# Kernel tuning notes

Hardware: AMD Instinct MI355X
Metric: run time of the kernel (lower is better)

## Reference

```python
import jax, jax.numpy as jnp
import numpy as np

N = 2048; E = 65536; T = 6; F_IN = 2
H_ENC = 256; LAT = 128; H_DEC = 256
PRED = 6
MIN_X, MAX_X = 0.0, 1.0
MIN_Y, MAX_Y = 0.0, 1.0
MIN_EW, MAX_EW = 0.0, 0.5
VISUAL_RANGE = 0.5


def setup_inputs() -> dict:
    key = jax.random.key(0)
    ks = jax.random.split(key, 17)
    p = lambda k, shape: jax.random.normal(k, shape, jnp.float32) * 0.05
    return {
        "x_seq": jax.random.uniform(ks[0], (T, N, F_IN), jnp.float32),
        "edge_index_seq": jax.random.randint(ks[1], (T, 2, E), 0, N),
        "edge_weight_seq": jax.random.uniform(ks[2], (T, E), jnp.float32, 1e-3, 1.0),
        "h_enc": jnp.zeros((N, H_ENC), jnp.float32),
        "h_dec": jnp.zeros((N, H_DEC), jnp.float32),
        "enc_Wx": p(ks[3], (3, 2, F_IN, H_ENC)),
        "enc_bx": p(ks[4], (3, H_ENC)),
        "enc_Wh": p(ks[5], (3, 2, H_ENC, H_ENC)),
        "enc_bh": p(ks[6], (3, H_ENC)),
        "enc_lin_W": p(ks[7], (H_ENC, LAT)),
        "enc_lin_b": p(ks[8], (LAT,)),
        "dec_Wx": p(ks[9], (3, 2, LAT, H_DEC)),
        "dec_bx": p(ks[10], (3, H_DEC)),
        "dec_Wh": p(ks[11], (3, 2, H_DEC, H_DEC)),
        "dec_bh": p(ks[12], (3, H_DEC)),
        "dec_lin_W": p(ks[13], (H_DEC, F_IN)),
        "dec_lin_b": p(ks[14], (F_IN,)),
    }


def _sparse_conv_fn(edge_index, edge_weight, n):
    # ChebConv K=2, sym normalization, lambda_max=2 => T1(L_hat) = -D^-1/2 A D^-1/2
    src, dst = edge_index[0], edge_index[1]
    deg = jax.ops.segment_sum(edge_weight, src, num_segments=n)
    dinv = jnp.where(deg > 0, jax.lax.rsqrt(jnp.where(deg > 0, deg, 1.0)), 0.0)
    norm = -dinv[src] * edge_weight * dinv[dst]  # [E]

    def conv(x, W, b):  # W: [2, in, out]
        tx1 = jax.ops.segment_sum(norm[:, None] * x[src], dst, num_segments=n)
        return x @ W[0] + tx1 @ W[1] + b
    return conv


def _dense_conv_fn(y_hat):
    # graph rebuilt from detached predicted coords (radius graph, dense masked form)
    c = jax.lax.stop_gradient(y_hat)
    px = c[:, 0] * (MAX_X - MIN_X) + MIN_X
    py = c[:, 1] * (MAX_Y - MIN_Y) + MIN_Y
    coords = jnp.stack((px, py), axis=1)  # [N, 2]
    d = jnp.linalg.norm(coords[:, None, :] - coords[None, :, :], axis=2)  # [N, N]
    mask = (d < VISUAL_RANGE) & (d > 0)
    w = jnp.where(mask, (d - MIN_EW) / (MAX_EW - MIN_EW), 0.0)
    deg = w.sum(axis=1)
    dinv = jnp.where(deg > 0, jax.lax.rsqrt(jnp.where(deg > 0, deg, 1.0)), 0.0)
    M = -(dinv[:, None] * w) * dinv[None, :]  # scaled-Laplacian off-diagonal

    def conv(x, W, b):
        return x @ W[0] + (M @ x) @ W[1] + b
    return conv


def _gru(conv, x, H, Wx, bx, Wh, bh):
    # GConvGRU gates: each gate = conv_x(X) + conv_h(H)
    z = jax.nn.sigmoid(conv(x, Wx[0], bx[0]) + conv(H, Wh[0], bh[0]))
    r = jax.nn.sigmoid(conv(x, Wx[1], bx[1]) + conv(H, Wh[1], bh[1]))
    h_tilde = jnp.tanh(conv(x, Wx[2], bx[2]) + conv(H * r, Wh[2], bh[2]))
    return z * H + (1.0 - z) * h_tilde


def reference(x_seq, edge_index_seq, edge_weight_seq, h_enc, h_dec,
              enc_Wx, enc_bx, enc_Wh, enc_bh, enc_lin_W, enc_lin_b,
              dec_Wx, dec_bx, dec_Wh, dec_bh, dec_lin_W, dec_lin_b):
    n = x_seq.shape[1]

    def step(conv, x, he, hd):
        he0 = _gru(conv, x, he, enc_Wx, enc_bx, enc_Wh, enc_bh)
        z = jax.nn.relu(he0) @ enc_lin_W + enc_lin_b
        hd0 = _gru(conv, z, hd, dec_Wx, dec_bx, dec_Wh, dec_bh)
        y_hat = jax.nn.relu(hd0) @ dec_lin_W + dec_lin_b
        return y_hat, he0, hd0

    # observed snapshots (sparse edge-list graphs)
    for t in range(x_seq.shape[0]):
        conv = _sparse_conv_fn(edge_index_seq[t], edge_weight_seq[t], n)
        y_hat, h_enc, h_dec = step(conv, x_seq[t], h_enc, h_dec)

    preds = [y_hat]
    for _ in range(PRED - 1):
        conv = _dense_conv_fn(y_hat)
        y_hat, h_enc, h_dec = step(conv, y_hat, h_enc, h_dec)
        preds.append(y_hat)
    return jnp.stack(preds)  # [PRED, N, 2]
```

## Files before the change

kernel.cpp:

```cpp
#include <hip/hip_runtime.h>
#include <math.h>

#define NN 2048
#define EE 65536
#define T_OBS 6
#define FIN 2
#define HE 256
#define LT 128
#define PREDN 6
#define DMM_NZ 8
#define ZR_NZ 4
#define GT_NZ 8
#define LIN_NZ 8

typedef __attribute__((ext_vector_type(8))) short short8v;
typedef __attribute__((ext_vector_type(4))) float float4v;

static __device__ __forceinline__ unsigned short f2bf(float f) {
    union { float f; unsigned u; } v; v.f = f;
    unsigned r = v.u + 0x7fff + ((v.u >> 16) & 1);
    return (unsigned short)(r >> 16);
}

static __device__ __forceinline__ void bfsplit(float f, unsigned short& h,
                                               unsigned short& l) {
    unsigned u = __float_as_uint(f);
    h = (unsigned short)(u >> 16);
    float hf = __uint_as_float(u & 0xffff0000u);
    l = (unsigned short)(__float_as_uint(f - hf) >> 16);
}

static __device__ __forceinline__ float bf2f(unsigned short b) {
    return __uint_as_float(((unsigned)b) << 16);
}

__global__ void k_degcnt_b(const int* __restrict__ ei, const float* __restrict__ ews,
                           float* __restrict__ deg_all, int* __restrict__ cnt_all) {
    int t = blockIdx.y;
    int e = blockIdx.x * blockDim.x + threadIdx.x;
    const int* src = ei + (size_t)t * 2 * EE;
    const int* dst = src + EE;
    const float* ew = ews + (size_t)t * EE;
    if (e < EE) {
        atomicAdd(&deg_all[t * NN + src[e]], ew[e]);
        atomicAdd(&cnt_all[t * NN + dst[e]], 1);
    }
}

__global__ void k_scan_b(const int* __restrict__ cnt_all, const float* __restrict__ deg_all,
                         int* __restrict__ roff_all, int* __restrict__ cur_all,
                         float* __restrict__ dinv_all) {
    __shared__ int part[256];
    int tg = blockIdx.x;
    const int* cnt = cnt_all + tg * NN;
    const float* deg = deg_all + tg * NN;
    int* roff = roff_all + tg * (NN + 1);
    int* cur = cur_all + tg * NN;
    float* dinv = dinv_all + tg * NN;
    int t = threadIdx.x;
#pragma unroll
    for (int i = t; i < NN; i += 256) {
        float d = deg[i];
        dinv[i] = d > 0.f ? 1.f / sqrtf(d) : 0.f;
    }
    int loc[8];
    int s = 0;
#pragma unroll
    for (int i = 0; i < 8; i++) { loc[i] = cnt[t * 8 + i]; s += loc[i]; }
    part[t] = s;
    __syncthreads();
    for (int off = 1; off < 256; off <<= 1) {
        int v = (t >= off) ? part[t - off] : 0;
        __syncthreads();
        part[t] += v;
        __syncthreads();
    }
    int run = (t == 0) ? 0 : part[t - 1];
#pragma unroll
    for (int i = 0; i < 8; i++) {
        int idx = t * 8 + i;
        roff[idx] = run;
        cur[idx] = run;
        run += loc[i];
    }
    if (t == 255) roff[NN] = run;
}

__global__ void k_scatter2_b(const int* __restrict__ ei, const float* __restrict__ ews,
                             const float* __restrict__ dinv_all, int* __restrict__ cur_all,
                             int* __restrict__ csr_src_all, float* __restrict__ csr_nrm_all) {
    int tg = blockIdx.y;
    int e = blockIdx.x * blockDim.x + threadIdx.x;
    const int* src = ei + (size_t)tg * 2 * EE;
    const int* dst = src + EE;
    const float* ew = ews + (size_t)tg * EE;
    const float* dinv = dinv_all + tg * NN;
    if (e < EE) {
        int s = src[e], d = dst[e];
        int p = atomicAdd(&cur_all[tg * NN + d], 1);
        csr_src_all[(size_t)tg * EE + p] = s;
        csr_nrm_all[(size_t)tg * EE + p] = -dinv[s] * ew[e] * dinv[d];
    }
}

__global__ void k_spmm2_b(const int* __restrict__ roff_all, const int* __restrict__ csr_src_all,
                          const float* __restrict__ csr_nrm_all, const float* __restrict__ x_seq,
                          float* __restrict__ aggx_all) {
    int tg = blockIdx.y;
    int nid = blockIdx.x * blockDim.x + threadIdx.x;
    if (nid < NN) {
        const int* roff = roff_all + tg * (NN + 1);
        const int* csr_src = csr_src_all + (size_t)tg * EE;
        const float* csr_nrm = csr_nrm_all + (size_t)tg * EE;
        const float* X = x_seq + (size_t)tg * NN * FIN;
        int s0 = roff[nid], s1 = roff[nid + 1];
        float a0 = 0.f, a1 = 0.f;
        for (int s = s0; s < s1; ++s) {
            int i = csr_src[s]; float w = csr_nrm[s];
            float2 xv = *(const float2*)&X[2 * i];
            a0 = fmaf(w, xv.x, a0);
            a1 = fmaf(w, xv.y, a1);
        }
        aggx_all[(size_t)tg * NN * FIN + 2 * nid] = a0;
        aggx_all[(size_t)tg * NN * FIN + 2 * nid + 1] = a1;
    }
}

template <int F>
__global__ void k_spmm_v(const int* __restrict__ roff, const int* __restrict__ csr_src,
                         const float* __restrict__ csr_nrm,
                         const float* __restrict__ X, float* __restrict__ out) {
    int w = threadIdx.x >> 6, lane = threadIdx.x & 63;
    int nid = (blockIdx.x << 2) + w;
    int c = lane << 2;
    int s0 = roff[nid], s1 = roff[nid + 1];
    float4 acc = make_float4(0.f, 0.f, 0.f, 0.f);
    int s = s0;
    for (; s + 8 <= s1; s += 8) {
        int is[8]; float ws[8];
#pragma unroll
        for (int j = 0; j < 8; j++) { is[j] = csr_src[s + j]; ws[j] = csr_nrm[s + j]; }
        if (c < F) {
            float4 xv[8];
#pragma unroll
            for (int j = 0; j < 8; j++) xv[j] = *(const float4*)&X[(size_t)is[j] * F + c];
#pragma unroll
            for (int j = 0; j < 8; j++) {
                acc.x = fmaf(ws[j], xv[j].x, acc.x);
                acc.y = fmaf(ws[j], xv[j].y, acc.y);
                acc.z = fmaf(ws[j], xv[j].z, acc.z);
                acc.w = fmaf(ws[j], xv[j].w, acc.w);
            }
        }
    }
    for (; s < s1; ++s) {
        int i0 = csr_src[s]; float w0 = csr_nrm[s];
        if (c < F) {
            float4 xv = *(const float4*)&X[(size_t)i0 * F + c];
            acc.x = fmaf(w0, xv.x, acc.x);
            acc.y = fmaf(w0, xv.y, acc.y);
            acc.z = fmaf(w0, xv.z, acc.z);
            acc.w = fmaf(w0, xv.w, acc.w);
        }
    }
    if (c < F) *(float4*)&out[(size_t)nid * F + c] = acc;
}

__global__ void k_ddeg(const float* __restrict__ c, float* __restrict__ dinv) {
    int i = blockIdx.x;
    int t = threadIdx.x;
    float xi = c[2 * i], yi = c[2 * i + 1];
    float s = 0.f;
    for (int j = t; j < NN; j += 256) {
        float dx = xi - c[2 * j], dy = yi - c[2 * j + 1];
        float d = sqrtf(dx * dx + dy * dy);
        if (d > 0.f && d < 0.5f) s += 2.f * d;
    }
    __shared__ float red[256];
    red[t] = s;
    __syncthreads();
    for (int off = 128; off > 0; off >>= 1) {
        if (t < off) red[t] += red[t + off];
        __syncthreads();
    }
    if (t == 0) {
        float d = red[0];
        dinv[i] = d > 0.f ? 1.f / sqrtf(d) : 0.f;
    }
}

__global__ void k_dM(const float* __restrict__ c, const float* __restrict__ dinv,
                     unsigned short* __restrict__ Mb) {
    int idx = blockIdx.x * blockDim.x + threadIdx.x;
    int i = idx >> 11, j = idx & (NN - 1);
    float dx = c[2 * i] - c[2 * j], dy = c[2 * i + 1] - c[2 * j + 1];
    float d = sqrtf(dx * dx + dy * dy);
    float w = (d > 0.f && d < 0.5f) ? 2.f * d : 0.f;
    Mb[idx] = f2bf(-(dinv[i] * w) * dinv[j]);
}

template <int F>
__global__ __launch_bounds__(256) void k_dmm_mf(
    const unsigned short* __restrict__ Mb, const float* __restrict__ X,
    float* __restrict__ pbuf)
{
    __shared__ __align__(16) unsigned short Ms[64][72];
    __shared__ __align__(16) unsigned short Xs[64][72];
    const int tid = threadIdx.x;
    const int wid = tid >> 6, lane = tid & 63;
    const int m0 = blockIdx.x << 6, n0 = blockIdx.y << 6;
    const int kb0 = blockIdx.z << 8;
    const int lr = lane & 15;
    const int kg = lane >> 4;
    float4v acc[4];
#pragma unroll
    for (int t = 0; t < 4; t++) acc[t] = (float4v){0.f, 0.f, 0.f, 0.f};

    for (int kb = kb0; kb < kb0 + 256; kb += 64) {
#pragma unroll
        for (int it = 0; it < 2; it++) {
            int i = tid + it * 256;
            int r = i >> 3, c8 = (i & 7) << 3;
            *(short8v*)&Ms[r][c8] =
                *(const short8v*)&Mb[(size_t)(m0 + r) * NN + kb + c8];
        }
#pragma unroll
        for (int it = 0; it < 2; it++) {
            int i = tid + it * 256;
            int k2 = (i & 31) << 1;
            int n4 = (i >> 5) << 2;
            float4 va = *(const float4*)&X[(size_t)(kb + k2) * F + n0 + n4];
            float4 vb = *(const float4*)&X[(size_t)(kb + k2 + 1) * F + n0 + n4];
            unsigned pk;
            pk = (unsigned)f2bf(va.x) | ((unsigned)f2bf(vb.x) << 16);
            *(unsigned*)&Xs[n4 + 0][k2] = pk;
            pk = (unsigned)f2bf(va.y) | ((unsigned)f2bf(vb.y) << 16);
            *(unsigned*)&Xs[n4 + 1][k2] = pk;
            pk = (unsigned)f2bf(va.z) | ((unsigned)f2bf(vb.z) << 16);
            *(unsigned*)&Xs[n4 + 2][k2] = pk;
            pk = (unsigned)f2bf(va.w) | ((unsigned)f2bf(vb.w) << 16);
            *(unsigned*)&Xs[n4 + 3][k2] = pk;
        }
        __syncthreads();
#pragma unroll
        for (int kh = 0; kh < 2; kh++) {
            int kk = kh * 32 + kg * 8;
            short8v a = *(const short8v*)&Ms[(wid << 4) + lr][kk];
#pragma unroll
            for (int t = 0; t < 4; t++) {
                short8v b = *(const short8v*)&Xs[(t << 4) + lr][kk];
                acc[t] = __builtin_amdgcn_mfma_f32_16x16x32_bf16(a, b, acc[t], 0, 0, 0);
            }
        }
        __syncthreads();
    }
    float* p = pbuf + (size_t)blockIdx.z * NN * F;
#pragma unroll
    for (int t = 0; t < 4; t++)
#pragma unroll
        for (int j = 0; j < 4; j++)
            p[(size_t)(m0 + (wid << 4) + (kg << 2) + j) * F + n0 + (t << 4) + lr] =
                acc[t][j];
}

template <int F, int NZ>
__global__ void k_redks(const float* __restrict__ pbuf, float* __restrict__ out) {
    const int TOT = NN * F / 4;
    int i = blockIdx.x * blockDim.x + threadIdx.x;
    if (i < TOT) {
        const float4* p = (const float4*)pbuf;
        float4 s = p[i];
#pragma unroll
        for (int z = 1; z < NZ; z++) {
            float4 v = p[(size_t)z * TOT + i];
            s.x += v.x; s.y += v.y; s.z += v.z; s.w += v.w;
        }
        ((float4*)out)[i] = s;
    }
}

__global__ void k_dmv2b(const unsigned short* __restrict__ Mb, const float* __restrict__ X,
                        float* __restrict__ out) {
    int i = blockIdx.x;
    int t = threadIdx.x;
    float a0 = 0.f, a1 = 0.f;
    for (int j = t; j < NN; j += 256) {
        float m = bf2f(Mb[(size_t)i * NN + j]);
        a0 = fmaf(m, X[2 * j], a0);
        a1 = fmaf(m, X[2 * j + 1], a1);
    }
    __shared__ float r0[256], r1[256];
    r0[t] = a0;
    r1[t] = a1;
    __syncthreads();
    for (int off = 128; off > 0; off >>= 1) {
        if (t < off) { r0[t] += r0[t + off]; r1[t] += r1[t + off]; }
        __syncthreads();
    }
    if (t == 0) { out[2 * i] = r0[0]; out[2 * i + 1] = r1[0]; }
}

template <bool RELU>
__device__ __forceinline__ void mfma_seg(
    unsigned short (*Ah)[40], unsigned short (*Al)[40],
    unsigned short (*Bh)[40], unsigned short (*Bl)[40],
    const float* __restrict__ A, int lda,
    const float* __restrict__ B, int ldb, int K,
    int m0, int tid, int wid, int lr, int kg, float4v (&acc)[4])
{
    for (int k0 = 0; k0 < K; k0 += 32) {
        {
            int r = tid >> 2, k8 = (tid & 3) << 3;
            const float* ap = &A[(size_t)(m0 + r) * lda + k0 + k8];
            float4 va = *(const float4*)ap;
            float4 vb = *(const float4*)(ap + 4);
            float v[8] = {va.x, va.y, va.z, va.w, vb.x, vb.y, vb.z, vb.w};
            short8v hv, lv;
#pragma unroll
            for (int j = 0; j < 8; j++) {
                float f = RELU ? fmaxf(v[j], 0.f) : v[j];
                unsigned short h, l;
                bfsplit(f, h, l);
                hv[j] = (short)h; lv[j] = (short)l;
            }
            *(short8v*)&Ah[r][k8] = hv;
            *(short8v*)&Al[r][k8] = lv;
        }
        {
            int k2 = (tid & 15) << 1;
            int n4 = (tid >> 4) << 2;
            const float* bp = &B[(size_t)(k0 + k2) * ldb + n4];
            float4 va = *(const float4*)bp;
            float4 vb = *(const float4*)(bp + ldb);
            float v0[4] = {va.x, va.y, va.z, va.w};
            float v1[4] = {vb.x, vb.y, vb.z, vb.w};
#pragma unroll
            for (int j = 0; j < 4; j++) {
                unsigned short h0, l0, h1, l1;
                bfsplit(v0[j], h0, l0);
                bfsplit(v1[j], h1, l1);
                *(unsigned*)&Bh[n4 + j][k2] = (unsigned)h0 | ((unsigned)h1 << 16);
                *(unsigned*)&Bl[n4 + j][k2] = (unsigned)l0 | ((unsigned)l1 << 16);
            }
        }
        __syncthreads();
        short8v ah = *(short8v*)&Ah[(wid << 4) + lr][kg << 3];
        short8v al = *(short8v*)&Al[(wid << 4) + lr][kg << 3];
#pragma unroll
        for (int t = 0; t < 4; t++) {
            short8v bh = *(short8v*)&Bh[(t << 4) + lr][kg << 3];
            short8v bl = *(short8v*)&Bl[(t << 4) + lr][kg << 3];
            acc[t] = __builtin_amdgcn_mfma_f32_16x16x32_bf16(ah, bh, acc[t], 0, 0, 0);
            acc[t] = __builtin_amdgcn_mfma_f32_16x16x32_bf16(ah, bl, acc[t], 0, 0, 0);
            acc[t] = __builtin_amdgcn_mfma_f32_16x16x32_bf16(al, bh, acc[t], 0, 0, 0);
        }
        __syncthreads();
    }
}

__global__ __launch_bounds__(256) void k_zr_ks(
    const float* __restrict__ A0, int K01, const float* __restrict__ A1,
    const float* __restrict__ H, const float* __restrict__ A3,
    const float* __restrict__ Wx, const float* __restrict__ Wh,
    float* __restrict__ pbuf)
{
    __shared__ __align__(16) unsigned short Ah[64][40], Al[64][40],
                                            Bh[64][40], Bl[64][40];
    int tid = threadIdx.x;
    int wid = tid >> 6, lane = tid & 63, lr = lane & 15, kg = lane >> 4;
    int m0 = blockIdx.x << 6;
    int g = blockIdx.y >> 2;
    int n0 = (blockIdx.y & 3) << 6;
    float4v acc[4];
#pragma unroll
    for (int t = 0; t < 4; t++) acc[t] = (float4v){0.f, 0.f, 0.f, 0.f};
    const float* As[4] = {A0, A1, H, A3};
    const int ldas[4] = {K01, K01, HE, HE};
    const float* Bs[4] = {
        Wx + (size_t)(g * 2 + 0) * K01 * HE + n0,
        Wx + (size_t)(g * 2 + 1) * K01 * HE + n0,
        Wh + (size_t)(g * 2 + 0) * HE * HE + n0,
        Wh + (size_t)(g * 2 + 1) * HE * HE + n0};
    const int Ks[4] = {K01, K01, HE, HE};
    int chunk = (2 * K01 + 2 * HE) / ZR_NZ;
    int lo = blockIdx.z * chunk, hi = lo + chunk;
    int off = 0;
#pragma unroll
    for (int s = 0; s < 4; s++) {
        int a = lo - off; a = a < 0 ? 0 : a;
        int b = hi - off; b = b > Ks[s] ? Ks[s] : b;
        if (b > a)
            mfma_seg<false>(Ah, Al, Bh, Bl, As[s] + a, ldas[s],
                            Bs[s] + (size_t)a * HE, HE, b - a,
                            m0, tid, wid, lr, kg, acc);
        off += Ks[s];
    }
    float* p = pbuf + (size_t)blockIdx.z * NN * 512;
    int cbase = (g << 8) + n0;
#pragma unroll
    for (int t = 0; t < 4; t++)
#pragma unroll
        for (int j = 0; j < 4; j++)
            p[(size_t)(m0 + (wid << 4) + (kg << 2) + j) * 512 + cbase + (t << 4) + lr] =
                acc[t][j];
}

__global__ void k_zr_ep(const float* __restrict__ pbuf,
                        const float* __restrict__ bx, const float* __restrict__ bh,
                        const float* __restrict__ H,
                        const float* __restrict__ x2, const float* __restrict__ ax2,
                        const float* __restrict__ Wx,
                        float* __restrict__ gz, float* __restrict__ hr)
{
    int i = blockIdx.x * 256 + threadIdx.x;
    const float4* p = (const float4*)pbuf;
    const size_t S = (size_t)NN * 512 / 4;
    float4 a = p[i];
#pragma unroll
    for (int z = 1; z < ZR_NZ; z++) {
        float4 v = p[(size_t)z * S + i];
        a.x += v.x; a.y += v.y; a.z += v.z; a.w += v.w;
    }
    int row = i >> 7, c = (i & 127) << 2;
    int g = c >> 8, cc = c & 255;
    if (Wx) {
        float x0 = x2[2 * row], x1 = x2[2 * row + 1];
        float q0 = ax2[2 * row], q1 = ax2[2 * row + 1];
        const float* W0 = Wx + (size_t)(g * 2 + 0) * FIN * HE;
        const float* W1 = Wx + (size_t)(g * 2 + 1) * FIN * HE;
        float4 w00 = *(const float4*)&W0[cc];
        float4 w01 = *(const float4*)&W0[HE + cc];
        float4 w10 = *(const float4*)&W1[cc];
        float4 w11 = *(const float4*)&W1[HE + cc];
        a.x += x0 * w00.x + x1 * w01.x + q0 * w10.x + q1 * w11.x;
        a.y += x0 * w00.y + x1 * w01.y + q0 * w10.y + q1 * w11.y;
        a.z += x0 * w00.z + x1 * w01.z + q0 * w10.z + q1 * w11.z;
        a.w += x0 * w00.w + x1 * w01.w + q0 * w10.w + q1 * w11.w;
    }
    float4 b0 = *(const float4*)&bx[c];
    float4 b1 = *(const float4*)&bh[c];
    float4 s;
    s.x = 1.f / (1.f + expf(-(a.x + b0.x + b1.x)));
    s.y = 1.f / (1.f + expf(-(a.y + b0.y + b1.y)));
    s.z = 1.f / (1.f + expf(-(a.z + b0.z + b1.z)));
    s.w = 1.f / (1.f + expf(-(a.w + b0.w + b1.w)));
    if (c < HE) {
        *(float4*)&gz[(size_t)row * HE + c] = s;
    } else {
        float4 h = *(const float4*)&H[(size_t)row * HE + cc];
        s.x *= h.x; s.y *= h.y; s.z *= h.z; s.w *= h.w;
        *(float4*)&hr[(size_t)row * HE + cc] = s;
    }
}

__global__ __launch_bounds__(256) void k_gt_ks(
    const float* __restrict__ A0, int K01, const float* __restrict__ A1,
    const float* __restrict__ hr, const float* __restrict__ A3,
    const float* __restrict__ Wx2, const float* __restrict__ Wh2,
    float* __restrict__ pbuf)
{
    __shared__ __align__(16) unsigned short Ah[64][40], Al[64][40],
                                            Bh[64][40], Bl[64][40];
    int tid = threadIdx.x;
    int wid = tid >> 6, lane = tid & 63, lr = lane & 15, kg = lane >> 4;
    int m0 = blockIdx.x << 6;
    int n0 = blockIdx.y << 6;
    float4v acc[4];
#pragma unroll
    for (int t = 0; t < 4; t++) acc[t] = (float4v){0.f, 0.f, 0.f, 0.f};
    const float* As[4] = {A0, A1, hr, A3};
    const int ldas[4] = {K01, K01, HE, HE};
    const float* Bs[4] = {
        Wx2 + n0,
        Wx2 + (size_t)K01 * HE + n0,
        Wh2 + n0,
        Wh2 + (size_t)HE * HE + n0};
    const int Ks[4] = {K01, K01, HE, HE};
    int chunk = (2 * K01 + 2 * HE) / GT_NZ;
    int lo = blockIdx.z * chunk, hi = lo + chunk;
    int off = 0;
#pragma unroll
    for (int s = 0; s < 4; s++) {
        int a = lo - off; a = a < 0 ? 0 : a;
        int b = hi - off; b = b > Ks[s] ? Ks[s] : b;
        if (b > a)
            mfma_seg<false>(Ah, Al, Bh, Bl, As[s] + a, ldas[s],
                            Bs[s] + (size_t)a * HE, HE, b - a,
                            m0, tid, wid, lr, kg, acc);
        off += Ks[s];
    }
    float* p = pbuf + (size_t)blockIdx.z * NN * HE;
#pragma unroll
    for (int t = 0; t < 4; t++)
#pragma unroll
        for (int j = 0; j < 4; j++)
            p[(size_t)(m0 + (wid << 4) + (kg << 2) + j) * HE + n0 + (t << 4) + lr] =
                acc[t][j];
}

__global__ void k_gt_ep(const float* __restrict__ pbuf,
                        const float* __restrict__ bx2, const float* __restrict__ bh2,
                        const float* __restrict__ gz,
                        const float* __restrict__ x2, const float* __restrict__ ax2,
                        const float* __restrict__ Wx2,
                        float* __restrict__ H)
{
    int i = blockIdx.x * 256 + threadIdx.x;
    const float4* p = (const float4*)pbuf;
    const size_t S = (size_t)NN * HE / 4;
    float4 a = p[i];
#pragma unroll
    for (int z = 1; z < GT_NZ; z++) {
        float4 v = p[(size_t)z * S + i];
        a.x += v.x; a.y += v.y; a.z += v.z; a.w += v.w;
    }
    int row = i >> 6, c = (i & 63) << 2;
    if (Wx2) {
        float x0 = x2[2 * row], x1 = x2[2 * row + 1];
        float q0 = ax2[2 * row], q1 = ax2[2 * row + 1];
        float4 w00 = *(const float4*)&Wx2[c];
        float4 w01 = *(const float4*)&Wx2[HE + c];
        float4 w10 = *(const float4*)&Wx2[2 * HE + c];
        float4 w11 = *(const float4*)&Wx2[3 * HE + c];
        a.x += x0 * w00.x + x1 * w01.x + q0 * w10.x + q1 * w11.x;
        a.y += x0 * w00.y + x1 * w01.y + q0 * w10.y + q1 * w11.y;
        a.z += x0 * w00.z + x1 * w01.z + q0 * w10.z + q1 * w11.z;
        a.w += x0 * w00.w + x1 * w01.w + q0 * w10.w + q1 * w11.w;
    }
    float4 b0 = *(const float4*)&bx2[c];
    float4 b1 = *(const float4*)&bh2[c];
    size_t idx = (size_t)row * HE + c;
    float4 z = *(const float4*)&gz[idx];
    float4 h = *(const float4*)&H[idx];
    float4 o;
    o.x = z.x * h.x + (1.f - z.x) * tanhf(a.x + b0.x + b1.x);
    o.y = z.y * h.y + (1.f - z.y) * tanhf(a.y + b0.y + b1.y);
    o.z = z.z * h.z + (1.f - z.z) * tanhf(a.z + b0.z + b1.z);
    o.w = z.w * h.w + (1.f - z.w) * tanhf(a.w + b0.w + b1.w);
    *(float4*)&H[idx] = o;
}

__global__ __launch_bounds__(256) void k_lin_ks(
    const float* __restrict__ A, const float* __restrict__ B,
    float* __restrict__ pbuf)
{
    __shared__ __align__(16) unsigned short Ah[64][40], Al[64][40],
                                            Bh[64][40], Bl[64][40];
    int tid = threadIdx.x;
    int wid = tid >> 6, lane = tid & 63, lr = lane & 15, kg = lane >> 4;
    int m0 = blockIdx.x << 6;
    int n0 = blockIdx.y << 6;
    int lo = blockIdx.z << 5;
    float4v acc[4];
#pragma unroll
    for (int t = 0; t < 4; t++) acc[t] = (float4v){0.f, 0.f, 0.f, 0.f};
    mfma_seg<true>(Ah, Al, Bh, Bl, A + lo, HE, B + (size_t)lo * LT + n0, LT, 32,
                   m0, tid, wid, lr, kg, acc);
    float* p = pbuf + (size_t)blockIdx.z * NN * LT;
#pragma unroll
    for (int t = 0; t < 4; t++)
#pragma unroll
        for (int j = 0; j < 4; j++)
            p[(size_t)(m0 + (wid << 4) + (kg << 2) + j) * LT + n0 + (t << 4) + lr] =
                acc[t][j];
}

__global__ void k_lin_ep(const float* __restrict__ pbuf,
                         const float* __restrict__ bias, float* __restrict__ out)
{
    int i = blockIdx.x * 256 + threadIdx.x;
    const float4* p = (const float4*)pbuf;
    const size_t S = (size_t)NN * LT / 4;
    int c = (i & 31) << 2;
    float4 bb = *(const float4*)&bias[c];
    float4 s = make_float4(bb.x, bb.y, bb.z, bb.w);
#pragma unroll
    for (int z = 0; z < LIN_NZ; z++) {
        float4 v = p[z * S + i];
        s.x += v.x; s.y += v.y; s.z += v.z; s.w += v.w;
    }
    ((float4*)out)[i] = s;
}

__global__ void k_declin(const float* __restrict__ A, const float* __restrict__ B,
                         const float* __restrict__ bias, float* __restrict__ out) {
    int w = threadIdx.x >> 6, lane = threadIdx.x & 63;
    int m = blockIdx.x * 4 + w;
    float4 a = *(const float4*)&A[(size_t)m * HE + (lane << 2)];
    float av[4] = {a.x, a.y, a.z, a.w};
    float a0 = 0.f, a1 = 0.f;
#pragma unroll
    for (int j = 0; j < 4; j++) {
        float v = fmaxf(av[j], 0.f);
        float2 b = *(const float2*)&B[((lane << 2) + j) * 2];
        a0 = fmaf(v, b.x, a0);
        a1 = fmaf(v, b.y, a1);
    }
    for (int off = 32; off > 0; off >>= 1) {
        a0 += __shfl_down(a0, off, 64);
        a1 += __shfl_down(a1, off, 64);
    }
    if (lane == 0) {
        out[2 * m] = a0 + bias[0];
        out[2 * m + 1] = a1 + bias[1];
    }
}

extern "C" void kernel_launch(void* const* d_in, const int* in_sizes, int n_in,
                              void* d_out, int out_size, void* d_ws, size_t ws_size,
                              hipStream_t stream) {
    (void)in_sizes; (void)n_in; (void)out_size; (void)ws_size;
    const float* x_seq = (const float*)d_in[0];
    const int* ei = (const int*)d_in[1];
    const float* ews = (const float*)d_in[2];
    const float* h_enc_in = (const float*)d_in[3];
    const float* h_dec_in = (const float*)d_in[4];
    const float* encWx = (const float*)d_in[5];
    const float* encbx = (const float*)d_in[6];
    const float* encWh = (const float*)d_in[7];
    const float* encbh = (const float*)d_in[8];
    const float* elinW = (const float*)d_in[9];
    const float* elinb = (const float*)d_in[10];
    const float* decWx = (const float*)d_in[11];
    const float* decbx = (const float*)d_in[12];
    const float* decWh = (const float*)d_in[13];
    const float* decbh = (const float*)d_in[14];
    const float* dlinW = (const float*)d_in[15];
    const float* dlinb = (const float*)d_in[16];
    float* out = (float*)d_out;

    float* W = (float*)d_ws;
    float* h_enc = W; W += (size_t)NN * HE;
    float* h_dec = W; W += (size_t)NN * HE;
    float* aggx  = W; W += (size_t)NN * HE;
    float* aggh  = W; W += (size_t)NN * HE;
    float* hr    = W; W += (size_t)NN * HE;
    float* agghr = W; W += (size_t)NN * HE;
    float* gz    = W; W += (size_t)NN * HE;
    float* zlat  = W; W += (size_t)NN * LT;
    float* yhat  = W; W += (size_t)NN * FIN;
    float* dinv_d = W; W += NN;
    unsigned short* Mb = (unsigned short*)W; W += (size_t)NN * NN / 2;
    float* pbuf  = W; W += (size_t)ZR_NZ * NN * 512;
    float* deg_all = W; W += (size_t)T_OBS * NN;
    int*   cnt_all = (int*)W; W += (size_t)T_OBS * NN;
    float* dinv_all = W; W += (size_t)T_OBS * NN;
    float* csr_nrm_all = W; W += (size_t)T_OBS * EE;
    float* aggx_all = W; W += (size_t)T_OBS * NN * FIN;
    int* roff_all = (int*)W; W += (size_t)T_OBS * (NN + 1) + 1;
    int* cur_all = (int*)W; W += (size_t)T_OBS * NN;
    int* csr_src_all = (int*)W; W += (size_t)T_OBS * EE;

    hipMemsetAsync(deg_all, 0, sizeof(float) * T_OBS * NN * 2, stream);
    k_degcnt_b<<<dim3(EE / 256, T_OBS), 256, 0, stream>>>(ei, ews, deg_all, cnt_all);
    k_scan_b<<<T_OBS, 256, 0, stream>>>(cnt_all, deg_all, roff_all, cur_all, dinv_all);
    k_scatter2_b<<<dim3(EE / 256, T_OBS), 256, 0, stream>>>(ei, ews, dinv_all, cur_all,
                                                            csr_src_all, csr_nrm_all);
    k_spmm2_b<<<dim3(NN / 256, T_OBS), 256, 0, stream>>>(roff_all, csr_src_all,
                                                         csr_nrm_all, x_seq, aggx_all);

    hipMemcpyAsync(h_enc, h_enc_in, sizeof(float) * NN * HE, hipMemcpyDeviceToDevice, stream);
    hipMemcpyAsync(h_dec, h_dec_in, sizeof(float) * NN * HE, hipMemcpyDeviceToDevice, stream);

    for (int step = 0; step < T_OBS + PREDN - 1; ++step) {
        bool sparse = step < T_OBS;
        const float* xin;
        const float* aggx_s;
        const int* roff = roff_all + step * (NN + 1);
        const int* csr_src = csr_src_all + (size_t)step * EE;
        const float* csr_nrm = csr_nrm_all + (size_t)step * EE;
        if (sparse) {
            xin = x_seq + (size_t)step * NN * FIN;
            aggx_s = aggx_all + (size_t)step * NN * FIN;
        } else {
            k_ddeg<<<NN, 256, 0, stream>>>(yhat, dinv_d);
            k_dM<<<(NN * NN) / 256, 256, 0, stream>>>(yhat, dinv_d, Mb);
            xin = yhat;
            k_dmv2b<<<NN, 256, 0, stream>>>(Mb, yhat, aggx);
            aggx_s = aggx;
        }

        if (sparse) {
            k_spmm_v<HE><<<NN / 4, 256, 0, stream>>>(roff, csr_src, csr_nrm, h_enc, aggh);
        } else {
            k_dmm_mf<HE><<<dim3(NN / 64, HE / 64, DMM_NZ), 256, 0, stream>>>(Mb, h_enc, pbuf);
            k_redks<HE, DMM_NZ><<<NN * HE / 4 / 256, 256, 0, stream>>>(pbuf, aggh);
        }
        k_zr_ks<<<dim3(NN / 64, 8, ZR_NZ), 256, 0, stream>>>(xin, 0, aggx_s, h_enc, aggh,
                                                             encWx, encWh, pbuf);
        k_zr_ep<<<NN * 512 / 4 / 256, 256, 0, stream>>>(pbuf, encbx, encbh, h_enc,
                                                        xin, aggx_s, encWx, gz, hr);
        if (sparse) {
            k_spmm_v<HE><<<NN / 4, 256, 0, stream>>>(roff, csr_src, csr_nrm, hr, agghr);
        } else {
            k_dmm_mf<HE><<<dim3(NN / 64, HE / 64, DMM_NZ), 256, 0, stream>>>(Mb, hr, pbuf);
            k_redks<HE, DMM_NZ><<<NN * HE / 4 / 256, 256, 0, stream>>>(pbuf, agghr);
        }
        k_gt_ks<<<dim3(NN / 64, 4, GT_NZ), 256, 0, stream>>>(xin, 0, aggx_s, hr, agghr,
                                                             encWx + 4 * FIN * HE,
                                                             encWh + 4 * HE * HE, pbuf);
        k_gt_ep<<<NN * HE / 4 / 256, 256, 0, stream>>>(pbuf, encbx + 2 * HE,
                                                       encbh + 2 * HE, gz,
                                                       xin, aggx_s, encWx + 4 * FIN * HE,
                                                       h_enc);
        k_lin_ks<<<dim3(NN / 64, 2, LIN_NZ), 256, 0, stream>>>(h_enc, elinW, pbuf);
        k_lin_ep<<<NN * LT / 4 / 256, 256, 0, stream>>>(pbuf, elinb, zlat);

        if (sparse) {
            k_spmm_v<LT><<<NN / 4, 256, 0, stream>>>(roff, csr_src, csr_nrm, zlat, aggx);
        } else {
            k_dmm_mf<LT><<<dim3(NN / 64, LT / 64, DMM_NZ), 256, 0, stream>>>(Mb, zlat, pbuf);
            k_redks<LT, DMM_NZ><<<NN * LT / 4 / 256, 256, 0, stream>>>(pbuf, aggx);
        }
        if (sparse) {
            k_spmm_v<HE><<<NN / 4, 256, 0, stream>>>(roff, csr_src, csr_nrm, h_dec, aggh);
        } else {
            k_dmm_mf<HE><<<dim3(NN / 64, HE / 64, DMM_NZ), 256, 0, stream>>>(Mb, h_dec, pbuf);
            k_redks<HE, DMM_NZ><<<NN * HE / 4 / 256, 256, 0, stream>>>(pbuf, aggh);
        }
        k_zr_ks<<<dim3(NN / 64, 8, ZR_NZ), 256, 0, stream>>>(zlat, LT, aggx, h_dec, aggh,
                                                             decWx, decWh, pbuf);
        k_zr_ep<<<NN * 512 / 4 / 256, 256, 0, stream>>>(pbuf, decbx, decbh, h_dec,
                                                        nullptr, nullptr, nullptr, gz, hr);
        if (sparse) {
            k_spmm_v<HE><<<NN / 4, 256, 0, stream>>>(roff, csr_src, csr_nrm, hr, agghr);
        } else {
            k_dmm_mf<HE><<<dim3(NN / 64, HE / 64, DMM_NZ), 256, 0, stream>>>(Mb, hr, pbuf);
            k_redks<HE, DMM_NZ><<<NN * HE / 4 / 256, 256, 0, stream>>>(pbuf, agghr);
        }
        k_gt_ks<<<dim3(NN / 64, 4, GT_NZ), 256, 0, stream>>>(zlat, LT, aggx, hr, agghr,
                                                             decWx + 4 * LT * HE,
                                                             decWh + 4 * HE * HE, pbuf);
        k_gt_ep<<<NN * HE / 4 / 256, 256, 0, stream>>>(pbuf, decbx + 2 * HE,
                                                       decbh + 2 * HE, gz,
                                                       nullptr, nullptr, nullptr,
                                                       h_dec);
        k_declin<<<NN / 4, 256, 0, stream>>>(h_dec, dlinW, dlinb, yhat);

        if (step >= T_OBS - 1) {
            hipMemcpyAsync(out + (size_t)(step - (T_OBS - 1)) * NN * FIN, yhat,
                           sizeof(float) * NN * FIN, hipMemcpyDeviceToDevice, stream);
        }
    }
}
```

Baseline: 1.742 ms.

## Store hidden states in bf16 shadow buffers and batch decoder aggregations

```diff
diff --git a/kernel.cpp b/kernel.cpp
--- a/kernel.cpp
+++ b/kernel.cpp
@@ -7,6 +7,7 @@
 #define FIN 2
 #define HE 256
 #define LT 128
+#define XC 384
 #define PREDN 6
 #define DMM_NZ 8
 #define ZR_NZ 4
@@ -14,6 +15,7 @@
 #define LIN_NZ 8
 
 typedef __attribute__((ext_vector_type(8))) short short8v;
+typedef __attribute__((ext_vector_type(4))) short short4v;
 typedef __attribute__((ext_vector_type(4))) float float4v;
 
 static __device__ __forceinline__ unsigned short f2bf(float f) {
@@ -34,16 +36,27 @@
     return __uint_as_float(((unsigned)b) << 16);
 }
 
-__global__ void k_degcnt_b(const int* __restrict__ ei, const float* __restrict__ ews,
-                           float* __restrict__ deg_all, int* __restrict__ cnt_all) {
-    int t = blockIdx.y;
-    int e = blockIdx.x * blockDim.x + threadIdx.x;
-    const int* src = ei + (size_t)t * 2 * EE;
+__global__ void k_degcnt_lds(const int* __restrict__ ei, const float* __restrict__ ews,
+                             float* __restrict__ deg_all, int* __restrict__ cnt_all) {
+    __shared__ float ldeg[NN];
+    __shared__ int lcnt[NN];
+    int tg = blockIdx.y;
+    const int* src = ei + (size_t)tg * 2 * EE;
     const int* dst = src + EE;
-    const float* ew = ews + (size_t)t * EE;
-    if (e < EE) {
-        atomicAdd(&deg_all[t * NN + src[e]], ew[e]);
-        atomicAdd(&cnt_all[t * NN + dst[e]], 1);
+    const float* ew = ews + (size_t)tg * EE;
+    for (int i = threadIdx.x; i < NN; i += 256) { ldeg[i] = 0.f; lcnt[i] = 0; }
+    __syncthreads();
+    const int EPB = EE / 8;
+    int e0 = blockIdx.x * EPB;
+    for (int e = e0 + threadIdx.x; e < e0 + EPB; e += 256) {
+        atomicAdd(&ldeg[src[e]], ew[e]);
+        atomicAdd(&lcnt[dst[e]], 1);
+    }
+    __syncthreads();
+    for (int i = threadIdx.x; i < NN; i += 256) {
+        float d = ldeg[i]; int cc = lcnt[i];
+        if (d != 0.f) atomicAdd(&deg_all[tg * NN + i], d);
+        if (cc) atomicAdd(&cnt_all[tg * NN + i], cc);
     }
 }
 
@@ -126,13 +139,15 @@
     }
 }
 
-template <int F>
-__global__ void k_spmm_v(const int* __restrict__ roff, const int* __restrict__ csr_src,
-                         const float* __restrict__ csr_nrm,
-                         const float* __restrict__ X, float* __restrict__ out) {
-    int w = threadIdx.x >> 6, lane = threadIdx.x & 63;
-    int nid = (blockIdx.x << 2) + w;
-    int c = lane << 2;
+template <int F, int TPN>
+__global__ void k_spmm_vb(const int* __restrict__ roff, const int* __restrict__ csr_src,
+                          const float* __restrict__ csr_nrm,
+                          const unsigned short* __restrict__ Xb,
+                          float* __restrict__ out, int ldo) {
+    const int NPB = 256 / TPN;
+    int w = threadIdx.x / TPN, l = threadIdx.x % TPN;
+    int nid = blockIdx.x * NPB + w;
+    int c = l << 2;
     int s0 = roff[nid], s1 = roff[nid + 1];
     float4 acc = make_float4(0.f, 0.f, 0.f, 0.f);
     int s = s0;
@@ -141,29 +156,30 @@
 #pragma unroll
         for (int j = 0; j < 8; j++) { is[j] = csr_src[s + j]; ws[j] = csr_nrm[s + j]; }
         if (c < F) {
-            float4 xv[8];
-#pragma unroll
-            for (int j = 0; j < 8; j++) xv[j] = *(const float4*)&X[(size_t)is[j] * F + c];
+            short4v xv[8];
+#pragma unroll
+            for (int j = 0; j < 8; j++)
+                xv[j] = *(const short4v*)&Xb[(size_t)is[j] * F + c];
 #pragma unroll
             for (int j = 0; j < 8; j++) {
-                acc.x = fmaf(ws[j], xv[j].x, acc.x);
-                acc.y = fmaf(ws[j], xv[j].y, acc.y);
-                acc.z = fmaf(ws[j], xv[j].z, acc.z);
-                acc.w = fmaf(ws[j], xv[j].w, acc.w);
+                acc.x = fmaf(ws[j], bf2f((unsigned short)xv[j][0]), acc.x);
+                acc.y = fmaf(ws[j], bf2f((unsigned short)xv[j][1]), acc.y);
+                acc.z = fmaf(ws[j], bf2f((unsigned short)xv[j][2]), acc.z);
+                acc.w = fmaf(ws[j], bf2f((unsigned short)xv[j][3]), acc.w);
             }
         }
     }
     for (; s < s1; ++s) {
         int i0 = csr_src[s]; float w0 = csr_nrm[s];
         if (c < F) {
-            float4 xv = *(const float4*)&X[(size_t)i0 * F + c];
-            acc.x = fmaf(w0, xv.x, acc.x);
-            acc.y = fmaf(w0, xv.y, acc.y);
-            acc.z = fmaf(w0, xv.z, acc.z);
-            acc.w = fmaf(w0, xv.w, acc.w);
-        }
-    }
-    if (c < F) *(float4*)&out[(size_t)nid * F + c] = acc;
+            short4v xv = *(const short4v*)&Xb[(size_t)i0 * F + c];
+            acc.x = fmaf(w0, bf2f((unsigned short)xv[0]), acc.x);
+            acc.y = fmaf(w0, bf2f((unsigned short)xv[1]), acc.y);
+            acc.z = fmaf(w0, bf2f((unsigned short)xv[2]), acc.z);
+            acc.w = fmaf(w0, bf2f((unsigned short)xv[3]), acc.w);
+        }
+    }
+    if (c < F) *(float4*)&out[(size_t)nid * ldo + c] = acc;
 }
 
 __global__ void k_ddeg(const float* __restrict__ c, float* __restrict__ dinv) {
@@ -189,19 +205,35 @@
     }
 }
 
-__global__ void k_dM(const float* __restrict__ c, const float* __restrict__ dinv,
-                     unsigned short* __restrict__ Mb) {
-    int idx = blockIdx.x * blockDim.x + threadIdx.x;
-    int i = idx >> 11, j = idx & (NN - 1);
-    float dx = c[2 * i] - c[2 * j], dy = c[2 * i + 1] - c[2 * j + 1];
-    float d = sqrtf(dx * dx + dy * dy);
-    float w = (d > 0.f && d < 0.5f) ? 2.f * d : 0.f;
-    Mb[idx] = f2bf(-(dinv[i] * w) * dinv[j]);
+__global__ void k_dM2(const float* __restrict__ c, const float* __restrict__ dinv,
+                      unsigned short* __restrict__ Mb, float* __restrict__ ax) {
+    int i = blockIdx.x;
+    int t = threadIdx.x;
+    float xi = c[2 * i], yi = c[2 * i + 1], di = dinv[i];
+    float a0 = 0.f, a1 = 0.f;
+    for (int j = t; j < NN; j += 256) {
+        float dx = xi - c[2 * j], dy = yi - c[2 * j + 1];
+        float d = sqrtf(dx * dx + dy * dy);
+        float w = (d > 0.f && d < 0.5f) ? 2.f * d : 0.f;
+        float v = -(di * w) * dinv[j];
+        Mb[(size_t)i * NN + j] = f2bf(v);
+        a0 = fmaf(v, c[2 * j], a0);
+        a1 = fmaf(v, c[2 * j + 1], a1);
+    }
+    __shared__ float r0[256], r1[256];
+    r0[t] = a0;
+    r1[t] = a1;
+    __syncthreads();
+    for (int off = 128; off > 0; off >>= 1) {
+        if (t < off) { r0[t] += r0[t + off]; r1[t] += r1[t + off]; }
+        __syncthreads();
+    }
+    if (t == 0) { ax[2 * i] = r0[0]; ax[2 * i + 1] = r1[0]; }
 }
 
 template <int F>
-__global__ __launch_bounds__(256) void k_dmm_mf(
-    const unsigned short* __restrict__ Mb, const float* __restrict__ X,
+__global__ __launch_bounds__(256) void k_dmm_mfb(
+    const unsigned short* __restrict__ Mb, const unsigned short* __restrict__ Xb,
     float* __restrict__ pbuf)
 {
     __shared__ __align__(16) unsigned short Ms[64][72];
@@ -229,17 +261,13 @@
             int i = tid + it * 256;
             int k2 = (i & 31) << 1;
             int n4 = (i >> 5) << 2;
-            float4 va = *(const float4*)&X[(size_t)(kb + k2) * F + n0 + n4];
-            float4 vb = *(const float4*)&X[(size_t)(kb + k2 + 1) * F + n0 + n4];
-            unsigned pk;
-            pk = (unsigned)f2bf(va.x) | ((unsigned)f2bf(vb.x) << 16);
-            *(unsigned*)&Xs[n4 + 0][k2] = pk;
-            pk = (unsigned)f2bf(va.y) | ((unsigned)f2bf(vb.y) << 16);
-            *(unsigned*)&Xs[n4 + 1][k2] = pk;
-            pk = (unsigned)f2bf(va.z) | ((unsigned)f2bf(vb.z) << 16);
-            *(unsigned*)&Xs[n4 + 2][k2] = pk;
-            pk = (unsigned)f2bf(va.w) | ((unsigned)f2bf(vb.w) << 16);
-            *(unsigned*)&Xs[n4 + 3][k2] = pk;
+            short4v va = *(const short4v*)&Xb[(size_t)(kb + k2) * F + n0 + n4];
+            short4v vb = *(const short4v*)&Xb[(size_t)(kb + k2 + 1) * F + n0 + n4];
+#pragma unroll
+            for (int j = 0; j < 4; j++)
+                *(unsigned*)&Xs[n4 + j][k2] =
+                    (unsigned)(unsigned short)va[j] |
+                    ((unsigned)(unsigned short)vb[j] << 16);
         }
         __syncthreads();
 #pragma unroll
@@ -277,27 +305,6 @@
         }
         ((float4*)out)[i] = s;
     }
-}
-
-__global__ void k_dmv2b(const unsigned short* __restrict__ Mb, const float* __restrict__ X,
-                        float* __restrict__ out) {
-    int i = blockIdx.x;
-    int t = threadIdx.x;
-    float a0 = 0.f, a1 = 0.f;
-    for (int j = t; j < NN; j += 256) {
-        float m = bf2f(Mb[(size_t)i * NN + j]);
-        a0 = fmaf(m, X[2 * j], a0);
-        a1 = fmaf(m, X[2 * j + 1], a1);
-    }
-    __shared__ float r0[256], r1[256];
-    r0[t] = a0;
-    r1[t] = a1;
-    __syncthreads();
-    for (int off = 128; off > 0; off >>= 1) {
-        if (t < off) { r0[t] += r0[t + off]; r1[t] += r1[t + off]; }
-        __syncthreads();
-    }
-    if (t == 0) { out[2 * i] = r0[0]; out[2 * i + 1] = r1[0]; }
 }
 
 template <bool RELU>
@@ -361,6 +368,7 @@
 __global__ __launch_bounds__(256) void k_zr_ks(
     const float* __restrict__ A0, int K01, const float* __restrict__ A1,
     const float* __restrict__ H, const float* __restrict__ A3,
+    int la1, int la2, int la3,
     const float* __restrict__ Wx, const float* __restrict__ Wh,
     float* __restrict__ pbuf)
 {
@@ -375,7 +383,7 @@
 #pragma unroll
     for (int t = 0; t < 4; t++) acc[t] = (float4v){0.f, 0.f, 0.f, 0.f};
     const float* As[4] = {A0, A1, H, A3};
-    const int ldas[4] = {K01, K01, HE, HE};
+    const int ldas[4] = {K01, la1, la2, la3};
     const float* Bs[4] = {
         Wx + (size_t)(g * 2 + 0) * K01 * HE + n0,
         Wx + (size_t)(g * 2 + 1) * K01 * HE + n0,
@@ -410,7 +418,8 @@
                         const float* __restrict__ H,
                         const float* __restrict__ x2, const float* __restrict__ ax2,
                         const float* __restrict__ Wx,
-                        float* __restrict__ gz, float* __restrict__ hr)
+                        float* __restrict__ gz, float* __restrict__ hr,
+                        unsigned short* __restrict__ hrb)
 {
     int i = blockIdx.x * 256 + threadIdx.x;
     const float4* p = (const float4*)pbuf;
@@ -447,15 +456,21 @@
     if (c < HE) {
         *(float4*)&gz[(size_t)row * HE + c] = s;
     } else {
-        float4 h = *(const float4*)&H[(size_t)row * HE + cc];
+        size_t idx = (size_t)row * HE + cc;
+        float4 h = *(const float4*)&H[idx];
         s.x *= h.x; s.y *= h.y; s.z *= h.z; s.w *= h.w;
-        *(float4*)&hr[(size_t)row * HE + cc] = s;
+        *(float4*)&hr[idx] = s;
+        short4v sb;
+        sb[0] = (short)f2bf(s.x); sb[1] = (short)f2bf(s.y);
+        sb[2] = (short)f2bf(s.z); sb[3] = (short)f2bf(s.w);
+        *(short4v*)&hrb[idx] = sb;
     }
 }
 
 __global__ __launch_bounds__(256) void k_gt_ks(
     const float* __restrict__ A0, int K01, const float* __restrict__ A1,
     const float* __restrict__ hr, const float* __restrict__ A3,
+    int la1, int la2, int la3,
     const float* __restrict__ Wx2, const float* __restrict__ Wh2,
     float* __restrict__ pbuf)
 {
@@ -469,7 +484,7 @@
 #pragma unroll
     for (int t = 0; t < 4; t++) acc[t] = (float4v){0.f, 0.f, 0.f, 0.f};
     const float* As[4] = {A0, A1, hr, A3};
-    const int ldas[4] = {K01, K01, HE, HE};
+    const int ldas[4] = {K01, la1, la2, la3};
     const float* Bs[4] = {
         Wx2 + n0,
         Wx2 + (size_t)K01 * HE + n0,
@@ -503,7 +518,8 @@
                         const float* __restrict__ gz,
                         const float* __restrict__ x2, const float* __restrict__ ax2,
                         const float* __restrict__ Wx2,
-                        float* __restrict__ H)
+                        float* __restrict__ H,
+                        unsigned short* __restrict__ Hb, int ldhb)
 {
     int i = blockIdx.x * 256 + threadIdx.x;
     const float4* p = (const float4*)pbuf;
@@ -538,6 +554,10 @@
     o.z = z.z * h.z + (1.f - z.z) * tanhf(a.z + b0.z + b1.z);
     o.w = z.w * h.w + (1.f - z.w) * tanhf(a.w + b0.w + b1.w);
     *(float4*)&H[idx] = o;
+    short4v sb;
+    sb[0] = (short)f2bf(o.x); sb[1] = (short)f2bf(o.y);
+    sb[2] = (short)f2bf(o.z); sb[3] = (short)f2bf(o.w);
+    *(short4v*)&Hb[(size_t)row * ldhb + c] = sb;
 }
 
 __global__ __launch_bounds__(256) void k_lin_ks(
@@ -566,12 +586,13 @@
 }
 
 __global__ void k_lin_ep(const float* __restrict__ pbuf,
-                         const float* __restrict__ bias, float* __restrict__ out)
+                         const float* __restrict__ bias, float* __restrict__ out,
+                         unsigned short* __restrict__ zb)
 {
     int i = blockIdx.x * 256 + threadIdx.x;
     const float4* p = (const float4*)pbuf;
     const size_t S = (size_t)NN * LT / 4;
-    int c = (i & 31) << 2;
+    int row = i >> 5, c = (i & 31) << 2;
     float4 bb = *(const float4*)&bias[c];
     float4 s = make_float4(bb.x, bb.y, bb.z, bb.w);
 #pragma unroll
@@ -580,6 +601,17 @@
         s.x += v.x; s.y += v.y; s.z += v.z; s.w += v.w;
     }
     ((float4*)out)[i] = s;
+    short4v sb;
+    sb[0] = (short)f2bf(s.x); sb[1] = (short)f2bf(s.y);
+    sb[2] = (short)f2bf(s.z); sb[3] = (short)f2bf(s.w);
+    *(short4v*)&zb[(size_t)row * XC + c] = sb;
+}
+
+__global__ void k_cvtb(const float* __restrict__ in, unsigned short* __restrict__ outb,
+                       int ldo) {
+    int i = blockIdx.x * 256 + threadIdx.x;
+    int r = i >> 8, c = i & 255;
+    outb[(size_t)r * ldo + c] = f2bf(in[i]);
 }
 
 __global__ void k_declin(const float* __restrict__ A, const float* __restrict__ B,
@@ -632,16 +664,20 @@
     float* W = (float*)d_ws;
     float* h_enc = W; W += (size_t)NN * HE;
     float* h_dec = W; W += (size_t)NN * HE;
-    float* aggx  = W; W += (size_t)NN * HE;
     float* aggh  = W; W += (size_t)NN * HE;
     float* hr    = W; W += (size_t)NN * HE;
     float* agghr = W; W += (size_t)NN * HE;
     float* gz    = W; W += (size_t)NN * HE;
     float* zlat  = W; W += (size_t)NN * LT;
+    float* Y     = W; W += (size_t)NN * XC;
     float* yhat  = W; W += (size_t)NN * FIN;
+    float* aggx2 = W; W += (size_t)NN * FIN;
     float* dinv_d = W; W += NN;
     unsigned short* Mb = (unsigned short*)W; W += (size_t)NN * NN / 2;
-    float* pbuf  = W; W += (size_t)ZR_NZ * NN * 512;
+    float* pbuf  = W; W += (size_t)DMM_NZ * NN * XC;
+    unsigned short* Hen_b = (unsigned short*)W; W += (size_t)NN * HE / 2;
+    unsigned short* hr_b  = (unsigned short*)W; W += (size_t)NN * HE / 2;
+    unsigned short* xcat_b = (unsigned short*)W; W += (size_t)NN * XC / 2;
     float* deg_all = W; W += (size_t)T_OBS * NN;
     int*   cnt_all = (int*)W; W += (size_t)T_OBS * NN;
     float* dinv_all = W; W += (size_t)T_OBS * NN;
@@ -652,7 +688,7 @@
     int* csr_src_all = (int*)W; W += (size_t)T_OBS * EE;
 
     hipMemsetAsync(deg_all, 0, sizeof(float) * T_OBS * NN * 2, stream);
-    k_degcnt_b<<<dim3(EE / 256, T_OBS), 256, 0, stream>>>(ei, ews, deg_all, cnt_all);
+    k_degcnt_lds<<<dim3(8, T_OBS), 256, 0, stream>>>(ei, ews, deg_all, cnt_all);
     k_scan_b<<<T_OBS, 256, 0, stream>>>(cnt_all, deg_all, roff_all, cur_all, dinv_all);
     k_scatter2_b<<<dim3(EE / 256, T_OBS), 256, 0, stream>>>(ei, ews, dinv_all, cur_all,
                                                             csr_src_all, csr_nrm_all);
@@ -661,6 +697,8 @@
 
     hipMemcpyAsync(h_enc, h_enc_in, sizeof(float) * NN * HE, hipMemcpyDeviceToDevice, stream);
     hipMemcpyAsync(h_dec, h_dec_in, sizeof(float) * NN * HE, hipMemcpyDeviceToDevice, stream);
+    k_cvtb<<<NN * HE / 256, 256, 0, stream>>>(h_enc_in, Hen_b, HE);
+    k_cvtb<<<NN * HE / 256, 256, 0, stream>>>(h_dec_in, xcat_b + LT, XC);
 
     for (int step = 0; step < T_OBS + PREDN - 1; ++step) {
         bool sparse = step < T_OBS;
@@ -674,67 +712,69 @@
             aggx_s = aggx_all + (size_t)step * NN * FIN;
         } else {
             k_ddeg<<<NN, 256, 0, stream>>>(yhat, dinv_d);
-            k_dM<<<(NN * NN) / 256, 256, 0, stream>>>(yhat, dinv_d, Mb);
+            k_dM2<<<NN, 256, 0, stream>>>(yhat, dinv_d, Mb, aggx2);
             xin = yhat;
-            k_dmv2b<<<NN, 256, 0, stream>>>(Mb, yhat, aggx);
-            aggx_s = aggx;
+            aggx_s = aggx2;
         }
 
         if (sparse) {
-            k_spmm_v<HE><<<NN / 4, 256, 0, stream>>>(roff, csr_src, csr_nrm, h_enc, aggh);
+            k_spmm_vb<HE, 64><<<NN / 4, 256, 0, stream>>>(roff, csr_src, csr_nrm,
+                                                          Hen_b, aggh, HE);
         } else {
-            k_dmm_mf<HE><<<dim3(NN / 64, HE / 64, DMM_NZ), 256, 0, stream>>>(Mb, h_enc, pbuf);
+            k_dmm_mfb<HE><<<dim3(NN / 64, HE / 64, DMM_NZ), 256, 0, stream>>>(Mb, Hen_b, pbuf);
             k_redks<HE, DMM_NZ><<<NN * HE / 4 / 256, 256, 0, stream>>>(pbuf, aggh);
         }
         k_zr_ks<<<dim3(NN / 64, 8, ZR_NZ), 256, 0, stream>>>(xin, 0, aggx_s, h_enc, aggh,
+                                                             FIN, HE, HE,
                                                              encWx, encWh, pbuf);
         k_zr_ep<<<NN * 512 / 4 / 256, 256, 0, stream>>>(pbuf, encbx, encbh, h_enc,
-                                                        xin, aggx_s, encWx, gz, hr);
+                                                        xin, aggx_s, encWx, gz, hr, hr_b);
         if (sparse) {
-            k_spmm_v<HE><<<NN / 4, 256, 0, stream>>>(roff, csr_src, csr_nrm, hr, agghr);
+            k_spmm_vb<HE, 64><<<NN / 4, 256, 0, stream>>>(roff, csr_src, csr_nrm,
+                                                          hr_b, agghr, HE);
         } else {
-            k_dmm_mf<HE><<<dim3(NN / 64, HE / 64, DMM_NZ), 256, 0, stream>>>(Mb, hr, pbuf);
+            k_dmm_mfb<HE><<<dim3(NN / 64, HE / 64, DMM_NZ), 256, 0, stream>>>(Mb, hr_b, pbuf);
             k_redks<HE, DMM_NZ><<<NN * HE / 4 / 256, 256, 0, stream>>>(pbuf, agghr);
         }
         k_gt_ks<<<dim3(NN / 64, 4, GT_NZ), 256, 0, stream>>>(xin, 0, aggx_s, hr, agghr,
+                                                             FIN, HE, HE,
                                                              encWx + 4 * FIN * HE,
                                                              encWh + 4 * HE * HE, pbuf);
         k_gt_ep<<<NN * HE / 4 / 256, 256, 0, stream>>>(pbuf, encbx + 2 * HE,
                                                        encbh + 2 * HE, gz,
                                                        xin, aggx_s, encWx + 4 * FIN * HE,
-                                                       h_enc);
+                                                       h_enc, Hen_b, HE);
         k_lin_ks<<<dim3(NN / 64, 2, LIN_NZ), 256, 0, stream>>>(h_enc, elinW, pbuf);
-        k_lin_ep<<<NN * LT / 4 / 256, 256, 0, stream>>>(pbuf, elinb, zlat);
+        k_lin_ep<<<NN * LT / 4 / 256, 256, 0, stream>>>(pbuf, elinb, zlat, xcat_b);
 
         if (sparse) {
-            k_spmm_v<LT><<<NN / 4, 256, 0, stream>>>(roff, csr_src, csr_nrm, zlat, aggx);
+            k_spmm_vb<XC, 128><<<NN / 2, 256, 0, stream>>>(roff, csr_src, csr_nrm,
+                                                           xcat_b, Y, XC);
         } else {
-            k_dmm_mf<LT><<<dim3(NN / 64, LT / 64, DMM_NZ), 256, 0, stream>>>(Mb, zlat, pbuf);
-            k_redks<LT, DMM_NZ><<<NN * LT / 4 / 256, 256, 0, stream>>>(pbuf, aggx);
-        }
-        if (sparse) {
-            k_spmm_v<HE><<<NN / 4, 256, 0, stream>>>(roff, csr_src, csr_nrm, h_dec, aggh);
-        } else {
-            k_dmm_mf<HE><<<dim3(NN / 64, HE / 64, DMM_NZ), 256, 0, stream>>>(Mb, h_dec, pbuf);
-            k_redks<HE, DMM_NZ><<<NN * HE / 4 / 256, 256, 0, stream>>>(pbuf, aggh);
-        }
-        k_zr_ks<<<dim3(NN / 64, 8, ZR_NZ), 256, 0, stream>>>(zlat, LT, aggx, h_dec, aggh,
+            k_dmm_mfb<XC><<<dim3(NN / 64, XC / 64, DMM_NZ), 256, 0, stream>>>(Mb, xcat_b, pbuf);
+            k_redks<XC, DMM_NZ><<<NN * XC / 4 / 256, 256, 0, stream>>>(pbuf, Y);
+        }
+        k_zr_ks<<<dim3(NN / 64, 8, ZR_NZ), 256, 0, stream>>>(zlat, LT, Y, h_dec, Y + LT,
+                                                             XC, HE, XC,
                                                              decWx, decWh, pbuf);
         k_zr_ep<<<NN * 512 / 4 / 256, 256, 0, stream>>>(pbuf, decbx, decbh, h_dec,
-                                                        nullptr, nullptr, nullptr, gz, hr);
+                                                        nullptr, nullptr, nullptr,
+                                                        gz, hr, hr_b);
         if (sparse) {
-            k_spmm_v<HE><<<NN / 4, 256, 0, stream>>>(roff, csr_src, csr_nrm, hr, agghr);
+            k_spmm_vb<HE, 64><<<NN / 4, 256, 0, stream>>>(roff, csr_src, csr_nrm,
+                                                          hr_b, agghr, HE);
         } else {
-            k_dmm_mf<HE><<<dim3(NN / 64, HE / 64, DMM_NZ), 256, 0, stream>>>(Mb, hr, pbuf);
+            k_dmm_mfb<HE><<<dim3(NN / 64, HE / 64, DMM_NZ), 256, 0, stream>>>(Mb, hr_b, pbuf);
             k_redks<HE, DMM_NZ><<<NN * HE / 4 / 256, 256, 0, stream>>>(pbuf, agghr);
         }
-        k_gt_ks<<<dim3(NN / 64, 4, GT_NZ), 256, 0, stream>>>(zlat, LT, aggx, hr, agghr,
+        k_gt_ks<<<dim3(NN / 64, 4, GT_NZ), 256, 0, stream>>>(zlat, LT, Y, hr, agghr,
+                                                             XC, HE, HE,
                                                              decWx + 4 * LT * HE,
                                                              decWh + 4 * HE * HE, pbuf);
         k_gt_ep<<<NN * HE / 4 / 256, 256, 0, stream>>>(pbuf, decbx + 2 * HE,
                                                        decbh + 2 * HE, gz,
                                                        nullptr, nullptr, nullptr,
-                                                       h_dec);
+                                                       h_dec, xcat_b + LT, XC);
         k_declin<<<NN / 4, 256, 0, stream>>>(h_dec, dlinW, dlinb, yhat);
 
         if (step >= T_OBS - 1) {
```

Result: faster. 1.655 ms (-5.0%).
